# Optimization experiments

Measured on AMD Instinct MI355X. Metric: run time of the kernel, lower is better.

Reference implementation:

```python
import jax, jax.numpy as jnp
import numpy as np

EPS = 1e-5  # nn.GroupNorm default


def setup_inputs() -> dict:
    key = jax.random.key(0)
    k1, k2, k3 = jax.random.split(key, 3)
    N, B, C, H, W = 8, 4, 256, 64, 64
    blocks = jax.random.normal(k1, (N, B, C, H, W), dtype=jnp.float32)
    x = jax.random.normal(k2, (B, C, H, W), dtype=jnp.float32)
    w = jax.random.normal(k3, (C,), dtype=jnp.float32) * 0.02
    gn_weight = jnp.ones((C,), dtype=jnp.float32)
    gn_bias = jnp.zeros((C,), dtype=jnp.float32)
    return {"blocks": blocks, "x": x, "w": w, "gn_weight": gn_weight, "gn_bias": gn_bias}


def reference(blocks, x, w, gn_weight, gn_bias):
    # V: [N1, B, C, H, W] = prior blocks + current features
    V = jnp.concatenate([blocks, x[None]], axis=0)
    # GroupNorm(1, C): normalize over (C, H, W) per (n, b) sample, per-channel affine
    mean = jnp.mean(V, axis=(2, 3, 4), keepdims=True)
    var = jnp.var(V, axis=(2, 3, 4), keepdims=True)
    K = (V - mean) * jax.lax.rsqrt(var + EPS)
    K = K * gn_weight[None, None, :, None, None] + gn_bias[None, None, :, None, None]
    # channel-dim dot product -> logits over depth blocks
    logits = jnp.einsum('c,nbchw->nbhw', w, K)
    attn = jax.nn.softmax(logits, axis=0)  # softmax over depth-block axis N1
    h = jnp.einsum('nbhw,nbchw->bchw', attn, V)
    return h
```

## Files before the change

### kernel.cpp

```cpp
#include <hip/hip_runtime.h>


#define NPRI 8
#define N1   9
#define BB   4
#define CC   256
#define HWN  4096
#define CHW  (CC * HWN)
#define NB   (N1 * BB)
#define GN_EPS 1e-5f

#define WS_SUM    0
#define WS_SQ     36
#define WS_SPART  128
#define WS_ATTN   589952

__global__ __launch_bounds__(256) void k1_stats(
        const float* __restrict__ blocks, const float* __restrict__ x,
        const float* __restrict__ w, const float* __restrict__ gnw,
        float* __restrict__ ws) {
    const int bid = blockIdx.x;
    const int nb  = bid >> 4;
    const int rem = bid & 15;
    const int cq  = rem >> 2;
    const int hwq = rem & 3;
    const int t   = threadIdx.x;

    const float* base = (nb < NPRI * BB)
        ? blocks + (size_t)nb * CHW
        : x + (size_t)(nb - NPRI * BB) * CHW;

    const int hw0 = hwq * 1024 + t * 4;
    float s0 = 0.f, s1 = 0.f, s2 = 0.f, s3 = 0.f;
    float sum = 0.f, sq = 0.f;
    const int c0 = cq * 64;

    #pragma unroll 8
    for (int c = c0; c < c0 + 64; ++c) {
        const float4 v = *reinterpret_cast<const float4*>(base + (size_t)c * HWN + hw0);
        const float wg = w[c] * gnw[c];
        sum += v.x + v.y + v.z + v.w;
        sq  += v.x * v.x + v.y * v.y + v.z * v.z + v.w * v.w;
        s0 += wg * v.x; s1 += wg * v.y; s2 += wg * v.z; s3 += wg * v.w;
    }

    float* Sp = ws + WS_SPART;
    *reinterpret_cast<float4*>(Sp + (size_t)(cq * NB + nb) * HWN + hw0) =
        make_float4(s0, s1, s2, s3);

    #pragma unroll
    for (int off = 32; off; off >>= 1) {
        sum += __shfl_down(sum, off);
        sq  += __shfl_down(sq, off);
    }
    __shared__ float red[8];
    const int wave = t >> 6, lane = t & 63;
    if (lane == 0) { red[wave] = sum; red[4 + wave] = sq; }
    __syncthreads();
    if (t == 0) {
        const float S = red[0] + red[1] + red[2] + red[3];
        const float Q = red[4] + red[5] + red[6] + red[7];
        atomicAdd(ws + WS_SUM + nb, S);
        atomicAdd(ws + WS_SQ + nb, Q);
    }
}

__global__ __launch_bounds__(256) void k2_attn(
        const float* __restrict__ w, const float* __restrict__ gnw,
        const float* __restrict__ gnb, float* __restrict__ ws) {
    const int t = threadIdx.x;

    float p = w[t] * gnw[t];
    float q = w[t] * gnb[t];
    #pragma unroll
    for (int off = 32; off; off >>= 1) {
        p += __shfl_down(p, off);
        q += __shfl_down(q, off);
    }
    __shared__ float red[8];
    __shared__ float swg_s, swgb_s;
    const int wave = t >> 6, lane = t & 63;
    if (lane == 0) { red[wave] = p; red[4 + wave] = q; }
    __syncthreads();
    if (t == 0) {
        swg_s  = red[0] + red[1] + red[2] + red[3];
        swgb_s = red[4] + red[5] + red[6] + red[7];
    }
    __syncthreads();
    const float swg = swg_s, swgb = swgb_s;

    const int idx = blockIdx.x * 256 + t;
    const int b  = idx >> 12;
    const int hw = idx & 4095;

    const float* Sp = ws + WS_SPART;
    float* attn = ws + WS_ATTN;

    float logit[N1];
    float mx = -1e30f;
    #pragma unroll
    for (int n = 0; n < N1; ++n) {
        const int nb = n * BB + b;
        const size_t o = (size_t)nb * HWN + hw;
        const float S = Sp[o] + Sp[(size_t)NB * HWN + o]
                      + Sp[(size_t)2 * NB * HWN + o] + Sp[(size_t)3 * NB * HWN + o];
        const float sum = ws[WS_SUM + nb];
        const float sq  = ws[WS_SQ + nb];
        const float mean = sum * (1.0f / CHW);
        const float var  = sq * (1.0f / CHW) - mean * mean;
        const float rstd = rsqrtf(var + GN_EPS);
        const float l = rstd * (S - mean * swg) + swgb;
        logit[n] = l;
        mx = fmaxf(mx, l);
    }
    float denom = 0.f;
    #pragma unroll
    for (int n = 0; n < N1; ++n) {
        const float e = __expf(logit[n] - mx);
        logit[n] = e;
        denom += e;
    }
    const float inv = 1.0f / denom;
    #pragma unroll
    for (int n = 0; n < N1; ++n)
        attn[(size_t)(n * BB + b) * HWN + hw] = logit[n] * inv;
}

__global__ __launch_bounds__(256) void k3_out(
        const float* __restrict__ blocks, const float* __restrict__ x,
        const float* __restrict__ ws, float* __restrict__ out) {
    const int bid = blockIdx.x;
    const int hwq = bid & 3;
    const int c   = (bid >> 2) & (CC - 1);
    const int b   = bid >> 10;
    const int t   = threadIdx.x;
    const int hw0 = hwq * 1024 + t * 4;

    const float* attn = ws + WS_ATTN;
    float a0 = 0.f, a1 = 0.f, a2 = 0.f, a3 = 0.f;

    #pragma unroll
    for (int n = 0; n < N1; ++n) {
        const float* vbase = (n < NPRI)
            ? blocks + ((size_t)(n * BB + b) * CC + c) * HWN
            : x + ((size_t)b * CC + c) * HWN;
        const float4 v = *reinterpret_cast<const float4*>(vbase + hw0);
        const float4 a = *reinterpret_cast<const float4*>(
            attn + (size_t)(n * BB + b) * HWN + hw0);
        a0 += a.x * v.x; a1 += a.y * v.y; a2 += a.z * v.z; a3 += a.w * v.w;
    }
    *reinterpret_cast<float4*>(out + ((size_t)(b * CC + c)) * HWN + hw0) =
        make_float4(a0, a1, a2, a3);
}

extern "C" void kernel_launch(void* const* d_in, const int* in_sizes, int n_in,
                              void* d_out, int out_size, void* d_ws, size_t ws_size,
                              hipStream_t stream) {
    const float* blocks = (const float*)d_in[0];
    const float* x      = (const float*)d_in[1];
    const float* w      = (const float*)d_in[2];
    const float* gnw    = (const float*)d_in[3];
    const float* gnb    = (const float*)d_in[4];
    float* out = (float*)d_out;
    float* ws  = (float*)d_ws;

    hipMemsetAsync(ws, 0, 72 * sizeof(float), stream);

    hipLaunchKernelGGL(k1_stats, dim3(576), dim3(256), 0, stream, blocks, x, w, gnw, ws);
    hipLaunchKernelGGL(k2_attn, dim3(64), dim3(256), 0, stream, w, gnw, gnb, ws);
    hipLaunchKernelGGL(k3_out, dim3(4096), dim3(256), 0, stream, blocks, x, ws, out);
}
```

Measured before the change: 64.63 us.

## Split stats pass across more blocks, drop atomics and memset, nontemporal output stores

The stats kernel now launches twice as many blocks, each covering half the hw range, with the two thread halves splitting channels and combining their partial dot sums through shared memory. Per-sample sum and sum-of-squares are written to per-block slots instead of atomics, which removes the memset launch; the attention kernel reduces those slots into shared mean/rstd tables once per block. The output kernel writes with nontemporal scalar stores. The aim is better occupancy on the bandwidth-bound read pass and less launch overhead, at the cost of an extra shared-memory sync, and the scalar stores may not merge as cleanly as the float4 store.

```diff
diff --git a/kernel.cpp b/kernel.cpp
--- a/kernel.cpp
+++ b/kernel.cpp
@@ -10,33 +10,35 @@
 #define NB   (N1 * BB)
 #define GN_EPS 1e-5f
 
-#define WS_SUM    0
-#define WS_SQ     36
-#define WS_SPART  128
-#define WS_ATTN   589952
+#define WS_PSUM   0
+#define WS_PSQ    1152
+#define WS_SPART  2304
+#define WS_ATTN   592128
 
 __global__ __launch_bounds__(256) void k1_stats(
         const float* __restrict__ blocks, const float* __restrict__ x,
         const float* __restrict__ w, const float* __restrict__ gnw,
         float* __restrict__ ws) {
     const int bid = blockIdx.x;
-    const int nb  = bid >> 4;
-    const int rem = bid & 15;
-    const int cq  = rem >> 2;
-    const int hwq = rem & 3;
+    const int nb  = bid >> 5;
+    const int cq  = (bid >> 3) & 3;
+    const int hwh = bid & 7;
     const int t   = threadIdx.x;
+    const int half = t >> 7;
+    const int tl   = t & 127;
 
     const float* base = (nb < NPRI * BB)
         ? blocks + (size_t)nb * CHW
         : x + (size_t)(nb - NPRI * BB) * CHW;
 
-    const int hw0 = hwq * 1024 + t * 4;
+    const int hw0 = hwh * 512 + tl * 4;
+    const int c0  = cq * 64 + half * 32;
+
     float s0 = 0.f, s1 = 0.f, s2 = 0.f, s3 = 0.f;
     float sum = 0.f, sq = 0.f;
-    const int c0 = cq * 64;
 
     #pragma unroll 8
-    for (int c = c0; c < c0 + 64; ++c) {
+    for (int c = c0; c < c0 + 32; ++c) {
         const float4 v = *reinterpret_cast<const float4*>(base + (size_t)c * HWN + hw0);
         const float wg = w[c] * gnw[c];
         sum += v.x + v.y + v.z + v.w;
@@ -44,9 +46,15 @@
         s0 += wg * v.x; s1 += wg * v.y; s2 += wg * v.z; s3 += wg * v.w;
     }
 
-    float* Sp = ws + WS_SPART;
-    *reinterpret_cast<float4*>(Sp + (size_t)(cq * NB + nb) * HWN + hw0) =
-        make_float4(s0, s1, s2, s3);
+    __shared__ float4 sbuf[128];
+    if (half) sbuf[tl] = make_float4(s0, s1, s2, s3);
+    __syncthreads();
+    if (!half) {
+        const float4 o = sbuf[tl];
+        float* Sp = ws + WS_SPART;
+        *reinterpret_cast<float4*>(Sp + (size_t)(cq * NB + nb) * HWN + hw0) =
+            make_float4(s0 + o.x, s1 + o.y, s2 + o.z, s3 + o.w);
+    }
 
     #pragma unroll
     for (int off = 32; off; off >>= 1) {
@@ -58,10 +66,9 @@
     if (lane == 0) { red[wave] = sum; red[4 + wave] = sq; }
     __syncthreads();
     if (t == 0) {
-        const float S = red[0] + red[1] + red[2] + red[3];
-        const float Q = red[4] + red[5] + red[6] + red[7];
-        atomicAdd(ws + WS_SUM + nb, S);
-        atomicAdd(ws + WS_SQ + nb, Q);
+        const int slot = nb * 32 + (bid & 31);
+        ws[WS_PSUM + slot] = red[0] + red[1] + red[2] + red[3];
+        ws[WS_PSQ  + slot] = red[4] + red[5] + red[6] + red[7];
     }
 }
 
@@ -70,6 +77,10 @@
         const float* __restrict__ gnb, float* __restrict__ ws) {
     const int t = threadIdx.x;
 
+    __shared__ float red[8];
+    __shared__ float swg_s, swgb_s;
+    __shared__ float mean_s[NB], rstd_s[NB];
+
     float p = w[t] * gnw[t];
     float q = w[t] * gnb[t];
     #pragma unroll
@@ -77,10 +88,21 @@
         p += __shfl_down(p, off);
         q += __shfl_down(q, off);
     }
-    __shared__ float red[8];
-    __shared__ float swg_s, swgb_s;
     const int wave = t >> 6, lane = t & 63;
     if (lane == 0) { red[wave] = p; red[4 + wave] = q; }
+
+    if (t < NB) {
+        float s = 0.f, ss = 0.f;
+        #pragma unroll 8
+        for (int i = 0; i < 32; ++i) {
+            s  += ws[WS_PSUM + t * 32 + i];
+            ss += ws[WS_PSQ  + t * 32 + i];
+        }
+        const float mean = s * (1.0f / CHW);
+        const float var  = ss * (1.0f / CHW) - mean * mean;
+        mean_s[t] = mean;
+        rstd_s[t] = rsqrtf(var + GN_EPS);
+    }
     __syncthreads();
     if (t == 0) {
         swg_s  = red[0] + red[1] + red[2] + red[3];
@@ -104,12 +126,7 @@
         const size_t o = (size_t)nb * HWN + hw;
         const float S = Sp[o] + Sp[(size_t)NB * HWN + o]
                       + Sp[(size_t)2 * NB * HWN + o] + Sp[(size_t)3 * NB * HWN + o];
-        const float sum = ws[WS_SUM + nb];
-        const float sq  = ws[WS_SQ + nb];
-        const float mean = sum * (1.0f / CHW);
-        const float var  = sq * (1.0f / CHW) - mean * mean;
-        const float rstd = rsqrtf(var + GN_EPS);
-        const float l = rstd * (S - mean * swg) + swgb;
+        const float l = rstd_s[nb] * (S - mean_s[nb] * swg) + swgb;
         logit[n] = l;
         mx = fmaxf(mx, l);
     }
@@ -149,8 +166,11 @@
             attn + (size_t)(n * BB + b) * HWN + hw0);
         a0 += a.x * v.x; a1 += a.y * v.y; a2 += a.z * v.z; a3 += a.w * v.w;
     }
-    *reinterpret_cast<float4*>(out + ((size_t)(b * CC + c)) * HWN + hw0) =
-        make_float4(a0, a1, a2, a3);
+    float* optr = out + ((size_t)(b * CC + c)) * HWN + hw0;
+    __builtin_nontemporal_store(a0, optr + 0);
+    __builtin_nontemporal_store(a1, optr + 1);
+    __builtin_nontemporal_store(a2, optr + 2);
+    __builtin_nontemporal_store(a3, optr + 3);
 }
 
 extern "C" void kernel_launch(void* const* d_in, const int* in_sizes, int n_in,
@@ -164,9 +184,7 @@
     float* out = (float*)d_out;
     float* ws  = (float*)d_ws;
 
-    hipMemsetAsync(ws, 0, 72 * sizeof(float), stream);
-
-    hipLaunchKernelGGL(k1_stats, dim3(576), dim3(256), 0, stream, blocks, x, w, gnw, ws);
+    hipLaunchKernelGGL(k1_stats, dim3(1152), dim3(256), 0, stream, blocks, x, w, gnw, ws);
     hipLaunchKernelGGL(k2_attn, dim3(64), dim3(256), 0, stream, w, gnw, gnb, ws);
     hipLaunchKernelGGL(k3_out, dim3(4096), dim3(256), 0, stream, blocks, x, ws, out);
 }
```

Result: faster. 61.64 us (-4.6%).
